# Optimization experiments

Hardware: AMD Instinct MI355X
Metric: run time of the kernel (lower is better)

## Reference

```python
import jax, jax.numpy as jnp
import numpy as np

VOCAB, D, H, L = 32000, 1024, 1024, 2
S, B = 512, 32
PAD = 1  # onmt.Constants.PAD -> embedding row zeroed


def setup_inputs() -> dict:
    key = jax.random.key(0)
    ks = jax.random.split(key, 12)
    sc = 0.05
    tokens = jax.random.randint(ks[0], (S, B), 0, VOCAB)
    h0 = jax.random.normal(ks[1], (L, B, H), jnp.float32)
    c0 = jax.random.normal(ks[2], (L, B, H), jnp.float32)
    emb = (jax.random.normal(ks[3], (VOCAB, D), jnp.float32) * sc).at[PAD].set(0.0)
    W_ih_0 = jax.random.normal(ks[4], (4 * H, D), jnp.float32) * sc
    W_hh_0 = jax.random.normal(ks[5], (4 * H, H), jnp.float32) * sc
    b_ih_0 = jax.random.normal(ks[6], (4 * H,), jnp.float32) * sc
    b_hh_0 = jax.random.normal(ks[7], (4 * H,), jnp.float32) * sc
    W_ih_1 = jax.random.normal(ks[8], (4 * H, H), jnp.float32) * sc
    W_hh_1 = jax.random.normal(ks[9], (4 * H, H), jnp.float32) * sc
    b_ih_1 = jax.random.normal(ks[10], (4 * H,), jnp.float32) * sc
    b_hh_1 = jax.random.normal(ks[11], (4 * H,), jnp.float32) * sc
    return dict(tokens=tokens, h0=h0, c0=c0, emb=emb,
                W_ih_0=W_ih_0, W_hh_0=W_hh_0, b_ih_0=b_ih_0, b_hh_0=b_hh_0,
                W_ih_1=W_ih_1, W_hh_1=W_hh_1, b_ih_1=b_ih_1, b_hh_1=b_hh_1)


def _lstm_cell(x, h, c, W_ih, W_hh, b_ih, b_hh):
    # PyTorch LSTMCell: gates = x W_ih^T + b_ih + h W_hh^T + b_hh ; order i,f,g,o
    gates = x @ W_ih.T + b_ih + h @ W_hh.T + b_hh  # [B, 4H]
    i, f, g, o = jnp.split(gates, 4, axis=-1)
    i = jax.nn.sigmoid(i); f = jax.nn.sigmoid(f)
    g = jnp.tanh(g); o = jax.nn.sigmoid(o)
    c_new = f * c + i * g
    h_new = o * jnp.tanh(c_new)
    return h_new, c_new


def reference(tokens, h0, c0, emb,
              W_ih_0, W_hh_0, b_ih_0, b_hh_0,
              W_ih_1, W_hh_1, b_ih_1, b_hh_1):
    x = emb[tokens]  # [S, B, D] embedding lookup
    layer_params = ((W_ih_0, W_hh_0, b_ih_0, b_hh_0),
                    (W_ih_1, W_hh_1, b_ih_1, b_hh_1))

    def step(carry, x_t):
        h, c = carry  # each [L, B, H]
        inp = x_t
        hs, cs = [], []
        for l in range(L):  # fixed small layer loop (structurally distinct params)
            h_l, c_l = _lstm_cell(inp, h[l], c[l], *layer_params[l])
            inp = h_l  # dropout=0.0 -> identity between layers and on output
            hs.append(h_l); cs.append(c_l)
        return (jnp.stack(hs), jnp.stack(cs)), inp

    (hF, cF), outputs = jax.lax.scan(step, (h0, c0), x)
    return outputs, (hF, cF)  # outputs: [S, B, H]
```

## Files before the change

### kernel.cpp

```cpp
#include <hip/hip_runtime.h>


typedef __bf16 bf16x8 __attribute__((ext_vector_type(8)));
typedef unsigned short u16x8 __attribute__((ext_vector_type(8)));
typedef float f32x4 __attribute__((ext_vector_type(4)));

#define NSTEPS 512
#define TEAM   128
#define OUT_ELEMS 16777216
#define BH 32768

#define LDS_BYTES 149248
#define OFF_SC   131072
#define OFF_BIAS 147968
#define OFF_CST  148096
#define OFF_TOK  149120

__device__ __forceinline__ unsigned short f2b(float f) {
    unsigned int u = __float_as_uint(f);
    u += 0x7fffu + ((u >> 16) & 1u);
    return (unsigned short)(u >> 16);
}
__device__ __forceinline__ float sigm(float x) { return 1.0f / (1.0f + __expf(-x)); }

__device__ __forceinline__ bf16x8 cvt8(const float* p) {
    float4 a = *(const float4*)p;
    float4 b = *(const float4*)(p + 4);
    u16x8 r;
    r[0] = f2b(a.x); r[1] = f2b(a.y); r[2] = f2b(a.z); r[3] = f2b(a.w);
    r[4] = f2b(b.x); r[5] = f2b(b.y); r[6] = f2b(b.z); r[7] = f2b(b.w);
    return __builtin_bit_cast(bf16x8, r);
}

__device__ __forceinline__ bf16x8 ld_mall16(const unsigned short* p) {
    uint4 r;
    asm volatile("global_load_dwordx4 %0, %1, off sc0 sc1" : "=v"(r) : "v"(p));
    return __builtin_bit_cast(bf16x8, r);
}
__device__ __forceinline__ void st_mall2(unsigned short* p, unsigned int v) {
    asm volatile("global_store_short %0, %1, off sc0 sc1" :: "v"(p), "v"(v) : "memory");
}
__device__ __forceinline__ void wait_vm0() {
    asm volatile("s_waitcnt vmcnt(0)" ::: "memory");
}
__device__ __forceinline__ unsigned int flag_ld(const unsigned int* p) {
    return __hip_atomic_load(p, __ATOMIC_RELAXED, __HIP_MEMORY_SCOPE_AGENT);
}
__device__ __forceinline__ void flag_st(unsigned int* p, unsigned int v) {
    __hip_atomic_store(p, v, __ATOMIC_RELAXED, __HIP_MEMORY_SCOPE_AGENT);
}

extern "C" __global__ __launch_bounds__(256, 1)
void lstm_persist(const int* __restrict__ tokens,
                  const float* __restrict__ h0in,
                  const float* __restrict__ c0in,
                  const float* __restrict__ emb,
                  const float* __restrict__ Wih0,
                  const float* __restrict__ Whh0,
                  const float* __restrict__ bih0,
                  const float* __restrict__ bhh0,
                  const float* __restrict__ Wih1,
                  const float* __restrict__ Whh1,
                  const float* __restrict__ bih1,
                  const float* __restrict__ bhh1,
                  float* __restrict__ dout,
                  unsigned short* __restrict__ h0b,
                  unsigned short* __restrict__ h1b,
                  unsigned int* __restrict__ cnt,
                  int R)
{
    extern __shared__ char smem[];
    unsigned short* wfrag = (unsigned short*)smem;
    float* sc   = (float*)(smem + OFF_SC);
    float* bias = (float*)(smem + OFF_BIAS);
    float* cst  = (float*)(smem + OFF_CST);
    int*   toks = (int*)(smem + OFF_TOK);

    const int tid  = threadIdx.x;
    const int w    = tid >> 6;
    const int lane = tid & 63;
    const int lm   = lane & 15;
    const int lq   = lane >> 4;
    const int blk  = blockIdx.x;
    const bool tB  = (blk >= TEAM);
    const int bid  = tB ? blk - TEAM : blk;
    const int n0   = bid * 8;

    const float* Wih = tB ? Wih1 : Wih0;
    const float* Whh = tB ? Whh1 : Whh0;
    const float* bi  = tB ? bih1 : bih0;
    const float* bh  = tB ? bhh1 : bhh0;
    unsigned int* flagA = cnt;
    unsigned int* flagB = cnt + TEAM;
    unsigned int* myflag = (tB ? flagB : flagA) + bid;

    {
        int u = tid & 7, b = tid >> 3;
        int loff = tB ? BH : 0;
        unsigned short v = f2b(h0in[loff + b * 1024 + n0 + u]);
        st_mall2((tB ? h1b : h0b) + (size_t)(R - 1) * BH + b * 1024 + n0 + u, (unsigned int)v);
    }

    for (int t = tid; t < 8192; t += 256) {
        int chunk = t >> 6; int l = t & 63;
        int mat = chunk >> 6; int rem = chunk & 63;
        int nt = rem >> 5; int ks = rem & 31;
        int n = l & 15, q = l >> 4;
        int cl = nt * 16 + n;
        int grow = (cl >> 3) * 1024 + n0 + (cl & 7);
        const float* src = (mat ? Whh : Wih) + (size_t)grow * 1024 + ks * 32 + q * 8;
        *(bf16x8*)(wfrag + chunk * 512 + l * 8) = cvt8(src);
    }
    if (tid < 32) {
        int grow = (tid >> 3) * 1024 + n0 + (tid & 7);
        bias[tid] = bi[grow] + bh[grow];
    }
    {
        int u = tid & 7, b = tid >> 3;
        int loff = tB ? BH : 0;
        cst[b * 8 + u] = c0in[loff + b * 1024 + n0 + u];
    }
    wait_vm0();
    __syncthreads();
    if (tid == 0) flag_st(myflag, 1u);

    f32x4 acc[2][2];
    bf16x8 pre[2][8];
    bf16x8 sa[2][8];
    const f32x4 zero = {0.f, 0.f, 0.f, 0.f};

    for (int s = 0; s < NSTEPS; ++s) {
        const int slotPrev = (s + R - 1) % R;
        const int slotCur  = s % R;
        const unsigned short* hs;
        int preMat, strMat;

        if (!tB) {
            if (tid < 32) toks[tid] = tokens[s * 32 + tid];
            __syncthreads();
            #pragma unroll
            for (int mt = 0; mt < 2; ++mt) {
                const float* rowp = emb + (size_t)toks[mt * 16 + lm] * 1024 + lq * 8;
                #pragma unroll
                for (int i = 0; i < 8; ++i)
                    pre[mt][i] = cvt8(rowp + (w * 8 + i) * 32);
            }
            if (tid < TEAM) {
                unsigned int tgt = (unsigned int)(s + 1);
                while (flag_ld(&flagA[tid]) < tgt) __builtin_amdgcn_s_sleep(1);
            } else if (s >= R) {
                unsigned int tgt = (unsigned int)(s - R + 2);
                while (flag_ld(&flagB[tid - TEAM]) < tgt) __builtin_amdgcn_s_sleep(1);
            }
            __syncthreads();
            hs = h0b + (size_t)slotPrev * BH;  preMat = 0; strMat = 1;
        } else {
            if (tid < TEAM) {
                unsigned int tgt = (unsigned int)(s + 1);
                while (flag_ld(&flagB[tid]) < tgt) __builtin_amdgcn_s_sleep(1);
            }
            __syncthreads();
            const unsigned short* h1src = h1b + (size_t)slotPrev * BH;
            #pragma unroll
            for (int mt = 0; mt < 2; ++mt)
                #pragma unroll
                for (int i = 0; i < 8; ++i)
                    pre[mt][i] = ld_mall16(h1src + (mt * 16 + lm) * 1024 + (w * 8 + i) * 32 + lq * 8);
            if (tid < TEAM) {
                unsigned int tgt = (unsigned int)(s + 2);
                while (flag_ld(&flagA[tid]) < tgt) __builtin_amdgcn_s_sleep(1);
            }
            __syncthreads();
            hs = h0b + (size_t)slotCur * BH;  preMat = 1; strMat = 0;
        }

        #pragma unroll
        for (int mt = 0; mt < 2; ++mt)
            #pragma unroll
            for (int i = 0; i < 8; ++i)
                sa[mt][i] = ld_mall16(hs + (mt * 16 + lm) * 1024 + (w * 8 + i) * 32 + lq * 8);
        wait_vm0();

        acc[0][0] = zero; acc[0][1] = zero; acc[1][0] = zero; acc[1][1] = zero;

        #pragma unroll
        for (int i = 0; i < 8; ++i) {
            int ks = w * 8 + i;
            bf16x8 bp0 = *(const bf16x8*)(wfrag + ((preMat * 2 + 0) * 32 + ks) * 512 + lane * 8);
            bf16x8 bp1 = *(const bf16x8*)(wfrag + ((preMat * 2 + 1) * 32 + ks) * 512 + lane * 8);
            bf16x8 bs0 = *(const bf16x8*)(wfrag + ((strMat * 2 + 0) * 32 + ks) * 512 + lane * 8);
            bf16x8 bs1 = *(const bf16x8*)(wfrag + ((strMat * 2 + 1) * 32 + ks) * 512 + lane * 8);
            acc[0][0] = __builtin_amdgcn_mfma_f32_16x16x32_bf16(pre[0][i], bp0, acc[0][0], 0, 0, 0);
            acc[0][1] = __builtin_amdgcn_mfma_f32_16x16x32_bf16(pre[0][i], bp1, acc[0][1], 0, 0, 0);
            acc[1][0] = __builtin_amdgcn_mfma_f32_16x16x32_bf16(pre[1][i], bp0, acc[1][0], 0, 0, 0);
            acc[1][1] = __builtin_amdgcn_mfma_f32_16x16x32_bf16(pre[1][i], bp1, acc[1][1], 0, 0, 0);
            acc[0][0] = __builtin_amdgcn_mfma_f32_16x16x32_bf16(sa[0][i], bs0, acc[0][0], 0, 0, 0);
            acc[0][1] = __builtin_amdgcn_mfma_f32_16x16x32_bf16(sa[0][i], bs1, acc[0][1], 0, 0, 0);
            acc[1][0] = __builtin_amdgcn_mfma_f32_16x16x32_bf16(sa[1][i], bs0, acc[1][0], 0, 0, 0);
            acc[1][1] = __builtin_amdgcn_mfma_f32_16x16x32_bf16(sa[1][i], bs1, acc[1][1], 0, 0, 0);
        }

        #pragma unroll
        for (int mt = 0; mt < 2; ++mt) {
            #pragma unroll
            for (int nt = 0; nt < 2; ++nt) {
                f32x4 a = acc[mt][nt];
                int col = nt * 16 + lm;
                int rb = w * 32 + mt * 16 + lq * 4;
                sc[(rb + 0) * 33 + col] = a[0];
                sc[(rb + 1) * 33 + col] = a[1];
                sc[(rb + 2) * 33 + col] = a[2];
                sc[(rb + 3) * 33 + col] = a[3];
            }
        }
        __syncthreads();

        {
            int u = tid & 7, b = tid >> 3;
            float G[4];
            #pragma unroll
            for (int g = 0; g < 4; ++g) {
                int col = g * 8 + u;
                float v = bias[col];
                #pragma unroll
                for (int w2 = 0; w2 < 4; ++w2) v += sc[(w2 * 32 + b) * 33 + col];
                G[g] = v;
            }
            float ig = sigm(G[0]);
            float fg = sigm(G[1]);
            float gg = tanhf(G[2]);
            float og = sigm(G[3]);
            float cOld = cst[b * 8 + u];
            float cNew = fg * cOld + ig * gg;
            float hNew = og * tanhf(cNew);
            cst[b * 8 + u] = cNew;
            unsigned short hb = f2b(hNew);
            int off = b * 1024 + n0 + u;
            if (!tB) {
                st_mall2(h0b + (size_t)slotCur * BH + off, (unsigned int)hb);
                if (s == NSTEPS - 1) {
                    dout[OUT_ELEMS + off] = hNew;
                    dout[OUT_ELEMS + 2 * BH + off] = cNew;
                }
            } else {
                dout[(size_t)s * BH + off] = hNew;
                st_mall2(h1b + (size_t)slotCur * BH + off, (unsigned int)hb);
                if (s == NSTEPS - 1) {
                    dout[OUT_ELEMS + BH + off] = hNew;
                    dout[OUT_ELEMS + 3 * BH + off] = cNew;
                }
            }
        }
        wait_vm0();
        __syncthreads();
        if (tid == 0) flag_st(myflag, (unsigned int)(s + 2));
    }
}

extern "C" void kernel_launch(void* const* d_in, const int* in_sizes, int n_in,
                              void* d_out, int out_size, void* d_ws, size_t ws_size,
                              hipStream_t stream) {
    hipFuncSetAttribute((const void*)lstm_persist,
                        hipFuncAttributeMaxDynamicSharedMemorySize, LDS_BYTES);
    hipMemsetAsync(d_ws, 0, 4096, stream);

    const int* tokens = (const int*)d_in[0];
    const float* h0   = (const float*)d_in[1];
    const float* c0   = (const float*)d_in[2];
    const float* emb  = (const float*)d_in[3];
    const float* Wih0 = (const float*)d_in[4];
    const float* Whh0 = (const float*)d_in[5];
    const float* bih0 = (const float*)d_in[6];
    const float* bhh0 = (const float*)d_in[7];
    const float* Wih1 = (const float*)d_in[8];
    const float* Whh1 = (const float*)d_in[9];
    const float* bih1 = (const float*)d_in[10];
    const float* bhh1 = (const float*)d_in[11];

    long long avail = (long long)ws_size - 4096;
    long long r = avail / (2LL * BH * 2);
    int R = (int)(r > NSTEPS ? NSTEPS : r);
    if (R < 2) R = 2;

    unsigned int* cnt = (unsigned int*)d_ws;
    unsigned short* h0b = (unsigned short*)((char*)d_ws + 4096);
    unsigned short* h1b = h0b + (size_t)R * BH;

    lstm_persist<<<dim3(256), dim3(256), LDS_BYTES, stream>>>(
        tokens, h0, c0, emb, Wih0, Whh0, bih0, bhh0, Wih1, Whh1, bih1, bhh1,
        (float*)d_out, h0b, h1b, cnt, R);
}
```

Measured before the change: 5.164 ms.

## Restructure LSTM step sync: split MFMA phases, vectorized h stores, early flag signal

Layer-1 blocks now poll both dependency flags up front and overlap the h1 and h0 loads, running the input-side MFMAs while the recurrent loads are still in flight (partial vmcnt wait). h outputs are staged in LDS and written as one 16-byte store per batch row instead of per-element short stores. The flag is published right after those stores drain, before the fp32 output writes, which shortens the critical path between teams. Tokens are read directly instead of through LDS plus a barrier, polling is reorganized per wavefront, the scratch stride is padded to 36, and the bf16 conversion uses native casts. The extra barrier and LDS staging add some cost, and the flag ordering relative to other warps' stores needs care.

```diff
diff --git a/kernel.cpp b/kernel.cpp
--- a/kernel.cpp
+++ b/kernel.cpp
@@ -4,17 +4,18 @@
 typedef __bf16 bf16x8 __attribute__((ext_vector_type(8)));
 typedef unsigned short u16x8 __attribute__((ext_vector_type(8)));
 typedef float f32x4 __attribute__((ext_vector_type(4)));
+typedef unsigned int u32x4 __attribute__((ext_vector_type(4)));
 
 #define NSTEPS 512
 #define TEAM   128
 #define OUT_ELEMS 16777216
 #define BH 32768
 
-#define LDS_BYTES 149248
+#define LDS_BYTES 151168
 #define OFF_SC   131072
-#define OFF_BIAS 147968
-#define OFF_CST  148096
-#define OFF_TOK  149120
+#define OFF_BIAS 149504
+#define OFF_CST  149632
+#define OFF_HST  150656
 
 __device__ __forceinline__ unsigned short f2b(float f) {
     unsigned int u = __float_as_uint(f);
@@ -26,28 +27,38 @@
 __device__ __forceinline__ bf16x8 cvt8(const float* p) {
     float4 a = *(const float4*)p;
     float4 b = *(const float4*)(p + 4);
-    u16x8 r;
-    r[0] = f2b(a.x); r[1] = f2b(a.y); r[2] = f2b(a.z); r[3] = f2b(a.w);
-    r[4] = f2b(b.x); r[5] = f2b(b.y); r[6] = f2b(b.z); r[7] = f2b(b.w);
-    return __builtin_bit_cast(bf16x8, r);
+    bf16x8 r;
+    r[0] = (__bf16)a.x; r[1] = (__bf16)a.y; r[2] = (__bf16)a.z; r[3] = (__bf16)a.w;
+    r[4] = (__bf16)b.x; r[5] = (__bf16)b.y; r[6] = (__bf16)b.z; r[7] = (__bf16)b.w;
+    return r;
 }
 
 __device__ __forceinline__ bf16x8 ld_mall16(const unsigned short* p) {
-    uint4 r;
+    u32x4 r;
     asm volatile("global_load_dwordx4 %0, %1, off sc0 sc1" : "=v"(r) : "v"(p));
     return __builtin_bit_cast(bf16x8, r);
 }
+__device__ __forceinline__ void st_mall16(unsigned short* p, u32x4 v) {
+    asm volatile("global_store_dwordx4 %0, %1, off sc0 sc1" :: "v"(p), "v"(v) : "memory");
+}
 __device__ __forceinline__ void st_mall2(unsigned short* p, unsigned int v) {
     asm volatile("global_store_short %0, %1, off sc0 sc1" :: "v"(p), "v"(v) : "memory");
 }
 __device__ __forceinline__ void wait_vm0() {
     asm volatile("s_waitcnt vmcnt(0)" ::: "memory");
 }
+__device__ __forceinline__ void wait_vm16() {
+    asm volatile("s_waitcnt vmcnt(16)" ::: "memory");
+}
 __device__ __forceinline__ unsigned int flag_ld(const unsigned int* p) {
     return __hip_atomic_load(p, __ATOMIC_RELAXED, __HIP_MEMORY_SCOPE_AGENT);
 }
 __device__ __forceinline__ void flag_st(unsigned int* p, unsigned int v) {
     __hip_atomic_store(p, v, __ATOMIC_RELAXED, __HIP_MEMORY_SCOPE_AGENT);
+}
+__device__ __forceinline__ void poll2(const unsigned int* f, int lane, unsigned int tgt) {
+    while (flag_ld(f + lane) < tgt) __builtin_amdgcn_s_sleep(1);
+    while (flag_ld(f + 64 + lane) < tgt) __builtin_amdgcn_s_sleep(1);
 }
 
 extern "C" __global__ __launch_bounds__(256, 1)
@@ -74,7 +85,7 @@
     float* sc   = (float*)(smem + OFF_SC);
     float* bias = (float*)(smem + OFF_BIAS);
     float* cst  = (float*)(smem + OFF_CST);
-    int*   toks = (int*)(smem + OFF_TOK);
+    unsigned short* hst = (unsigned short*)(smem + OFF_HST);
 
     const int tid  = threadIdx.x;
     const int w    = tid >> 6;
@@ -136,29 +147,20 @@
         int preMat, strMat;
 
         if (!tB) {
-            if (tid < 32) toks[tid] = tokens[s * 32 + tid];
-            __syncthreads();
             #pragma unroll
             for (int mt = 0; mt < 2; ++mt) {
-                const float* rowp = emb + (size_t)toks[mt * 16 + lm] * 1024 + lq * 8;
+                const float* rowp = emb + (size_t)tokens[s * 32 + mt * 16 + lm] * 1024 + lq * 8;
                 #pragma unroll
                 for (int i = 0; i < 8; ++i)
                     pre[mt][i] = cvt8(rowp + (w * 8 + i) * 32);
             }
-            if (tid < TEAM) {
-                unsigned int tgt = (unsigned int)(s + 1);
-                while (flag_ld(&flagA[tid]) < tgt) __builtin_amdgcn_s_sleep(1);
-            } else if (s >= R) {
-                unsigned int tgt = (unsigned int)(s - R + 2);
-                while (flag_ld(&flagB[tid - TEAM]) < tgt) __builtin_amdgcn_s_sleep(1);
-            }
+            if (w == 0)                   poll2(flagA, lane, (unsigned int)(s + 1));
+            else if (w == 1 && s >= R)    poll2(flagB, lane, (unsigned int)(s - R + 2));
             __syncthreads();
             hs = h0b + (size_t)slotPrev * BH;  preMat = 0; strMat = 1;
         } else {
-            if (tid < TEAM) {
-                unsigned int tgt = (unsigned int)(s + 1);
-                while (flag_ld(&flagB[tid]) < tgt) __builtin_amdgcn_s_sleep(1);
-            }
+            if (w == 0)      poll2(flagB, lane, (unsigned int)(s + 1));
+            else if (w == 1) poll2(flagA, lane, (unsigned int)(s + 2));
             __syncthreads();
             const unsigned short* h1src = h1b + (size_t)slotPrev * BH;
             #pragma unroll
@@ -166,11 +168,6 @@
                 #pragma unroll
                 for (int i = 0; i < 8; ++i)
                     pre[mt][i] = ld_mall16(h1src + (mt * 16 + lm) * 1024 + (w * 8 + i) * 32 + lq * 8);
-            if (tid < TEAM) {
-                unsigned int tgt = (unsigned int)(s + 2);
-                while (flag_ld(&flagA[tid]) < tgt) __builtin_amdgcn_s_sleep(1);
-            }
-            __syncthreads();
             hs = h0b + (size_t)slotCur * BH;  preMat = 1; strMat = 0;
         }
 
@@ -179,21 +176,30 @@
             #pragma unroll
             for (int i = 0; i < 8; ++i)
                 sa[mt][i] = ld_mall16(hs + (mt * 16 + lm) * 1024 + (w * 8 + i) * 32 + lq * 8);
-        wait_vm0();
 
         acc[0][0] = zero; acc[0][1] = zero; acc[1][0] = zero; acc[1][1] = zero;
+
+        if (tB) { wait_vm16(); __builtin_amdgcn_sched_barrier(0); }
 
         #pragma unroll
         for (int i = 0; i < 8; ++i) {
             int ks = w * 8 + i;
             bf16x8 bp0 = *(const bf16x8*)(wfrag + ((preMat * 2 + 0) * 32 + ks) * 512 + lane * 8);
             bf16x8 bp1 = *(const bf16x8*)(wfrag + ((preMat * 2 + 1) * 32 + ks) * 512 + lane * 8);
-            bf16x8 bs0 = *(const bf16x8*)(wfrag + ((strMat * 2 + 0) * 32 + ks) * 512 + lane * 8);
-            bf16x8 bs1 = *(const bf16x8*)(wfrag + ((strMat * 2 + 1) * 32 + ks) * 512 + lane * 8);
             acc[0][0] = __builtin_amdgcn_mfma_f32_16x16x32_bf16(pre[0][i], bp0, acc[0][0], 0, 0, 0);
             acc[0][1] = __builtin_amdgcn_mfma_f32_16x16x32_bf16(pre[0][i], bp1, acc[0][1], 0, 0, 0);
             acc[1][0] = __builtin_amdgcn_mfma_f32_16x16x32_bf16(pre[1][i], bp0, acc[1][0], 0, 0, 0);
             acc[1][1] = __builtin_amdgcn_mfma_f32_16x16x32_bf16(pre[1][i], bp1, acc[1][1], 0, 0, 0);
+        }
+
+        wait_vm0();
+        __builtin_amdgcn_sched_barrier(0);
+
+        #pragma unroll
+        for (int i = 0; i < 8; ++i) {
+            int ks = w * 8 + i;
+            bf16x8 bs0 = *(const bf16x8*)(wfrag + ((strMat * 2 + 0) * 32 + ks) * 512 + lane * 8);
+            bf16x8 bs1 = *(const bf16x8*)(wfrag + ((strMat * 2 + 1) * 32 + ks) * 512 + lane * 8);
             acc[0][0] = __builtin_amdgcn_mfma_f32_16x16x32_bf16(sa[0][i], bs0, acc[0][0], 0, 0, 0);
             acc[0][1] = __builtin_amdgcn_mfma_f32_16x16x32_bf16(sa[0][i], bs1, acc[0][1], 0, 0, 0);
             acc[1][0] = __builtin_amdgcn_mfma_f32_16x16x32_bf16(sa[1][i], bs0, acc[1][0], 0, 0, 0);
@@ -207,10 +213,10 @@
                 f32x4 a = acc[mt][nt];
                 int col = nt * 16 + lm;
                 int rb = w * 32 + mt * 16 + lq * 4;
-                sc[(rb + 0) * 33 + col] = a[0];
-                sc[(rb + 1) * 33 + col] = a[1];
-                sc[(rb + 2) * 33 + col] = a[2];
-                sc[(rb + 3) * 33 + col] = a[3];
+                sc[(rb + 0) * 36 + col] = a[0];
+                sc[(rb + 1) * 36 + col] = a[1];
+                sc[(rb + 2) * 36 + col] = a[2];
+                sc[(rb + 3) * 36 + col] = a[3];
             }
         }
         __syncthreads();
@@ -223,7 +229,7 @@
                 int col = g * 8 + u;
                 float v = bias[col];
                 #pragma unroll
-                for (int w2 = 0; w2 < 4; ++w2) v += sc[(w2 * 32 + b) * 33 + col];
+                for (int w2 = 0; w2 < 4; ++w2) v += sc[(w2 * 32 + b) * 36 + col];
                 G[g] = v;
             }
             float ig = sigm(G[0]);
@@ -234,26 +240,31 @@
             float cNew = fg * cOld + ig * gg;
             float hNew = og * tanhf(cNew);
             cst[b * 8 + u] = cNew;
-            unsigned short hb = f2b(hNew);
+            hst[b * 8 + u] = f2b(hNew);
+            __syncthreads();
+
+            if (tid < 32) {
+                u32x4 v16 = *(const u32x4*)(hst + tid * 8);
+                unsigned short* dst = (tB ? h1b : h0b) + (size_t)slotCur * BH + tid * 1024 + n0;
+                st_mall16(dst, v16);
+            }
+            if (w == 0) {
+                wait_vm0();
+                if (tid == 0) flag_st(myflag, (unsigned int)(s + 2));
+            }
+
             int off = b * 1024 + n0 + u;
-            if (!tB) {
-                st_mall2(h0b + (size_t)slotCur * BH + off, (unsigned int)hb);
-                if (s == NSTEPS - 1) {
-                    dout[OUT_ELEMS + off] = hNew;
-                    dout[OUT_ELEMS + 2 * BH + off] = cNew;
-                }
-            } else {
+            if (tB) {
                 dout[(size_t)s * BH + off] = hNew;
-                st_mall2(h1b + (size_t)slotCur * BH + off, (unsigned int)hb);
                 if (s == NSTEPS - 1) {
                     dout[OUT_ELEMS + BH + off] = hNew;
                     dout[OUT_ELEMS + 3 * BH + off] = cNew;
                 }
-            }
-        }
-        wait_vm0();
-        __syncthreads();
-        if (tid == 0) flag_st(myflag, (unsigned int)(s + 2));
+            } else if (s == NSTEPS - 1) {
+                dout[OUT_ELEMS + off] = hNew;
+                dout[OUT_ELEMS + 2 * BH + off] = cNew;
+            }
+        }
     }
 }
 
```

Measured after the change: 4.605 ms. 10.8% less time.
